# Performance work log

Hardware: AMD Instinct MI355X
Metric: run time of the kernel (lower is better)

Reference implementation:

```python
import jax, jax.numpy as jnp
import numpy as np

IN_FEATURES = 1024
HIDDEN_DIM = 1024
B, S = 4, 4096


def setup_inputs() -> dict:
    key = jax.random.key(0)
    ks = jax.random.split(key, 7)
    lim = 1.0 / np.sqrt(IN_FEATURES)
    x = jax.random.normal(ks[0], (B, S, IN_FEATURES), dtype=jnp.float32)
    Wq = jax.random.uniform(ks[1], (IN_FEATURES, HIDDEN_DIM), jnp.float32, -lim, lim)
    bq = jax.random.uniform(ks[2], (HIDDEN_DIM,), jnp.float32, -lim, lim)
    Wk = jax.random.uniform(ks[3], (IN_FEATURES, HIDDEN_DIM), jnp.float32, -lim, lim)
    bk = jax.random.uniform(ks[4], (HIDDEN_DIM,), jnp.float32, -lim, lim)
    Wv = jax.random.uniform(ks[5], (IN_FEATURES, HIDDEN_DIM), jnp.float32, -lim, lim)
    bv = jax.random.uniform(ks[6], (HIDDEN_DIM,), jnp.float32, -lim, lim)
    return {"x": x, "Wq": Wq, "bq": bq, "Wk": Wk, "bk": bk, "Wv": Wv, "bv": bv}


def reference(x, Wq, bq, Wk, bk, Wv, bv):
    # QKV projections: [B, S, H]
    q = jnp.einsum('bsf,fh->bsh', x, Wq) + bq
    k = jnp.einsum('bsf,fh->bsh', x, Wk) + bk
    v = jnp.einsum('bsf,fh->bsh', x, Wv) + bv
    scale = 1.0 / jnp.sqrt(jnp.asarray(q.shape[-1], dtype=q.dtype))
    scores = jnp.einsum('bqh,bkh->bqk', q, k) * scale  # [B, S, S]
    weights = jax.nn.softmax(scores, axis=-1)
    return jnp.einsum('bqk,bkh->bqh', weights, v)
```

## Files before the change

kernel.cpp:

```cpp
#include <hip/hip_runtime.h>

typedef _Float16 half_t;
typedef _Float16 half4_t __attribute__((ext_vector_type(4)));
typedef _Float16 half8_t __attribute__((ext_vector_type(8)));
typedef float float4_t __attribute__((ext_vector_type(4)));

#define S_LEN 4096
#define NB 4
#define H_DIM 1024

#define MFMA16(a, b, c) __builtin_amdgcn_mfma_f32_16x16x32_f16(a, b, c, 0, 0, 0)

#define BAR_LDS()                                      \
  do {                                                 \
    asm volatile("s_waitcnt lgkmcnt(0)" ::: "memory"); \
    __builtin_amdgcn_s_barrier();                      \
  } while (0)

__global__ __launch_bounds__(256) void wt_prep(
    const float* __restrict__ Wq, const float* __restrict__ Wk,
    const float* __restrict__ Wv, half_t* __restrict__ wth,
    half_t* __restrict__ wtl) {
  const int zi = blockIdx.z;
  const float* W = (zi == 0) ? Wq : (zi == 1) ? Wk : Wv;
  half_t* oh = wth + (size_t)zi * H_DIM * H_DIM;
  half_t* ol = wtl + (size_t)zi * H_DIM * H_DIM;
  const int h0 = blockIdx.x * 32, f0 = blockIdx.y * 32;
  __shared__ float Ws[32][33];
  const int t = threadIdx.x;
  const int c = t & 31, r8 = t >> 5;
#pragma unroll
  for (int rr = 0; rr < 4; rr++)
    Ws[r8 * 4 + rr][c] = W[(size_t)(f0 + r8 * 4 + rr) * H_DIM + h0 + c];
  __syncthreads();
#pragma unroll
  for (int rr = 0; rr < 4; rr++) {
    int h = r8 * 4 + rr;
    float v = Ws[c][h];
    half_t hi = (half_t)v;
    half_t lo = (half_t)(v - (float)hi);
    oh[(size_t)(h0 + h) * H_DIM + f0 + c] = hi;
    ol[(size_t)(h0 + h) * H_DIM + f0 + c] = lo;
  }
}

#define QKV_BK 64

__global__ __launch_bounds__(512, 2) void qkv_mfma(
    const float* __restrict__ x, const half_t* __restrict__ wth,
    const half_t* __restrict__ wtl, const float* __restrict__ bq,
    const float* __restrict__ bk, const float* __restrict__ bv,
    half_t* __restrict__ ws) {
  const int bx = blockIdx.x;
  const int zi = bx >> 2;
  const int m0 = (bx & 3) * 256;
  const int n0 = blockIdx.y * 256;
  const half_t* Ah_g = wth + (size_t)zi * H_DIM * H_DIM;
  const half_t* Al_g = wtl + (size_t)zi * H_DIM * H_DIM;
  const float* bias = (zi == 0) ? bq : (zi == 1) ? bk : bv;
  half_t* out = ws + (size_t)zi * ((size_t)NB * S_LEN * H_DIM);
  const int t = threadIdx.x;
  const int w = t >> 6, lane = t & 63, ln = lane & 15, quad = lane >> 4;

  __shared__ half_t Bs[2][32768];

  float4_t acc[2][16] = {};

  const int ss = t >> 1;
  const int fh = (t & 1) * 32;
  const int snt = ss >> 4, sln = ss & 15;

  const float* xrow = x + (size_t)(n0 + ss) * H_DIM + fh;

  float4 xr[8];
#pragma unroll
  for (int g = 0; g < 4; g++) {
    xr[2 * g] = *(const float4*)(xrow + g * 8);
    xr[2 * g + 1] = *(const float4*)(xrow + g * 8 + 4);
  }
#pragma unroll
  for (int g = 0; g < 4; g++) {
    float vv[8] = {xr[2 * g].x,     xr[2 * g].y,     xr[2 * g].z,
                   xr[2 * g].w,     xr[2 * g + 1].x, xr[2 * g + 1].y,
                   xr[2 * g + 1].z, xr[2 * g + 1].w};
    half8_t hhi, hlo;
#pragma unroll
    for (int j = 0; j < 8; j++) {
      half_t h = (half_t)vv[j];
      hhi[j] = h;
      hlo[j] = (half_t)(vv[j] - (float)h);
    }
    int f = fh + g * 8;
    int k2 = f >> 5, qd = (f >> 3) & 3;
    int base = ((k2 * 16 + snt) * 64 + qd * 16 + sln) * 8;
    *(half8_t*)&Bs[0][base] = hhi;
    *(half8_t*)&Bs[0][16384 + base] = hlo;
  }

  for (int it = 0; it < 16; it++) {
    const int k0 = it * QKV_BK;
    const int cur = it & 1;
    const bool more = (it < 15);

    half8_t ah[2][2], al[2][2];
#pragma unroll
    for (int i = 0; i < 2; i++) {
      const size_t arow =
          (size_t)(m0 + w * 32 + i * 16 + ln) * H_DIM + k0 + quad * 8;
#pragma unroll
      for (int k2 = 0; k2 < 2; k2++) {
        ah[i][k2] = *(const half8_t*)(Ah_g + arow + k2 * 32);
        al[i][k2] = *(const half8_t*)(Al_g + arow + k2 * 32);
      }
    }
    if (more) {
      const float* xp = xrow + (k0 + QKV_BK);
#pragma unroll
      for (int g = 0; g < 4; g++) {
        xr[2 * g] = *(const float4*)(xp + g * 8);
        xr[2 * g + 1] = *(const float4*)(xp + g * 8 + 4);
      }
    }

    BAR_LDS();

#pragma unroll
    for (int k2 = 0; k2 < 2; k2++) {
#pragma unroll
      for (int nt = 0; nt < 16; nt++) {
        int base = ((k2 * 16 + nt) * 64 + lane) * 8;
        half8_t bh = *(const half8_t*)&Bs[cur][base];
        half8_t bl = *(const half8_t*)&Bs[cur][16384 + base];
        acc[0][nt] = MFMA16(ah[0][k2], bh, acc[0][nt]);
        acc[1][nt] = MFMA16(ah[1][k2], bh, acc[1][nt]);
        acc[0][nt] = MFMA16(al[0][k2], bh, acc[0][nt]);
        acc[1][nt] = MFMA16(al[1][k2], bh, acc[1][nt]);
        acc[0][nt] = MFMA16(ah[0][k2], bl, acc[0][nt]);
        acc[1][nt] = MFMA16(ah[1][k2], bl, acc[1][nt]);
      }
    }

    if (more) {
#pragma unroll
      for (int g = 0; g < 4; g++) {
        float vv[8] = {xr[2 * g].x,     xr[2 * g].y,     xr[2 * g].z,
                       xr[2 * g].w,     xr[2 * g + 1].x, xr[2 * g + 1].y,
                       xr[2 * g + 1].z, xr[2 * g + 1].w};
        half8_t hhi, hlo;
#pragma unroll
        for (int j = 0; j < 8; j++) {
          half_t h = (half_t)vv[j];
          hhi[j] = h;
          hlo[j] = (half_t)(vv[j] - (float)h);
        }
        int f = fh + g * 8;
        int k2 = f >> 5, qd = (f >> 3) & 3;
        int base = ((k2 * 16 + snt) * 64 + qd * 16 + sln) * 8;
        *(half8_t*)&Bs[cur ^ 1][base] = hhi;
        *(half8_t*)&Bs[cur ^ 1][16384 + base] = hlo;
      }
    }
  }

  const float oscale = (zi == 0) ? 0.03125f : 1.0f;
  float bb[2][4];
#pragma unroll
  for (int i = 0; i < 2; i++)
#pragma unroll
    for (int r = 0; r < 4; r++)
      bb[i][r] = bias[m0 + w * 32 + i * 16 + quad * 4 + r];

  if (zi < 2) {
#pragma unroll
    for (int i = 0; i < 2; i++)
#pragma unroll
      for (int nt = 0; nt < 16; nt++) {
        half4_t h4;
#pragma unroll
        for (int r = 0; r < 4; r++)
          h4[r] = (half_t)((acc[i][nt][r] + bb[i][r]) * oscale);
        size_t s = n0 + nt * 16 + ln;
        *(half4_t*)&out[s * H_DIM + m0 + w * 32 + i * 16 + quad * 4] = h4;
      }
  } else {
#pragma unroll
    for (int i = 0; i < 2; i++)
#pragma unroll
      for (int nt = 0; nt < 16; nt++) {
        int sf = n0 + nt * 16 + ln;
        int b = sf >> 12, si = sf & 4095;
#pragma unroll
        for (int r = 0; r < 4; r++) {
          int h = m0 + w * 32 + i * 16 + quad * 4 + r;
          out[((size_t)b * H_DIM + h) * S_LEN + si] =
              (half_t)(acc[i][nt][r] + bb[i][r]);
        }
      }
  }
}

#define TQ 64
#define TK 128

__global__ __launch_bounds__(512, 2) void flash_attn(
    const half_t* __restrict__ qw, const half_t* __restrict__ kw,
    const half_t* __restrict__ vt, float* __restrict__ out) {
  const int slot = blockIdx.x & 7;
  const int b = slot >> 1;
  const int qb = ((blockIdx.x >> 3) << 1) | (slot & 1);
  const int q0 = qb * TQ;
  const int t = threadIdx.x;
  const int w = t >> 6;
  const int lane = t & 63;
  const int ln = lane & 15;
  const int quad = lane >> 4;

  __shared__ half_t Qs[65536];
  __shared__ half_t Ps[8192];
  __shared__ float wmax[8][64];
  __shared__ float wl[8][64];

  const half_t* qp = qw + ((size_t)b * S_LEN + q0) * H_DIM;
  const half_t* kbp = kw + (size_t)b * S_LEN * H_DIM;
  const half_t* vbt = vt + (size_t)b * H_DIM * S_LEN;

  const half_t* kr = kbp + (size_t)(w * 16 + ln) * H_DIM + quad * 8;
  half8_t kbuf[6];
#pragma unroll
  for (int d = 0; d < 6; d++) kbuf[d] = *(const half8_t*)(kr + d * 32);

#pragma unroll
  for (int i = 0; i < 16; i++) {
    int flat = t * 8 + i * 4096;
    int r = flat >> 10, c = flat & 1023;
    int rs = r >> 4, lq = r & 15, ks = c >> 5, qd = (c >> 3) & 3;
    *(half8_t*)&Qs[((rs * 32 + ks) * 64 + qd * 16 + lq) * 8] =
        *(const half8_t*)&qp[(size_t)r * H_DIM + c];
  }
  BAR_LDS();

  float m_l = -1e30f;
  float l_l = 0.0f;

  float4_t O[4][8] = {};

  for (int kt = 0; kt < S_LEN; kt += TK) {
    float4_t s[4] = {};
    __builtin_amdgcn_s_setprio(1);
#pragma unroll
    for (int ks = 0; ks < 32; ks++) {
      half8_t a0 = *(const half8_t*)&Qs[(ks * 64 + lane) * 8];
      half8_t a1 = *(const half8_t*)&Qs[16384 + (ks * 64 + lane) * 8];
      half8_t a2 = *(const half8_t*)&Qs[32768 + (ks * 64 + lane) * 8];
      half8_t a3 = *(const half8_t*)&Qs[49152 + (ks * 64 + lane) * 8];
      half8_t kc = kbuf[ks % 6];
      if (ks < 26) kbuf[ks % 6] = *(const half8_t*)(kr + (ks + 6) * 32);
      s[0] = MFMA16(a0, kc, s[0]);
      s[1] = MFMA16(a1, kc, s[1]);
      s[2] = MFMA16(a2, kc, s[2]);
      s[3] = MFMA16(a3, kc, s[3]);
    }
    __builtin_amdgcn_s_setprio(0);

    kr += (size_t)TK * H_DIM;
    if (kt + TK < S_LEN) {
#pragma unroll
      for (int d = 0; d < 6; d++) kbuf[d] = *(const half8_t*)(kr + d * 32);
    }

    const half_t* vbase = vbt + (size_t)(w * 128 + ln) * S_LEN + kt + quad * 8;
    half8_t vr[4];
#pragma unroll
    for (int j = 0; j < 4; j++)
      vr[j] = *(const half8_t*)(vbase + (size_t)j * 16 * S_LEN);

    float rm[4][4];
#pragma unroll
    for (int rs = 0; rs < 4; rs++)
#pragma unroll
      for (int r = 0; r < 4; r++) rm[rs][r] = s[rs][r];
#pragma unroll
    for (int off = 1; off < 16; off <<= 1)
#pragma unroll
      for (int rs = 0; rs < 4; rs++)
#pragma unroll
        for (int r = 0; r < 4; r++)
          rm[rs][r] = fmaxf(rm[rs][r], __shfl_xor(rm[rs][r], off));
    if (ln == 0)
#pragma unroll
      for (int rs = 0; rs < 4; rs++)
#pragma unroll
        for (int r = 0; r < 4; r++)
          wmax[w][rs * 16 + quad * 4 + r] = rm[rs][r];
    BAR_LDS();

    float nm_l = m_l;
#pragma unroll
    for (int w2 = 0; w2 < 8; w2++) nm_l = fmaxf(nm_l, wmax[w2][lane]);
    float aS_l = __expf(m_l - nm_l);
    m_l = nm_l;

    const int pbase = (w >> 1) * 512 + (w & 1) * 256 + (ln >> 3) * 128 +
                      quad * 32 + (ln & 7);
    float pl[4][4];
#pragma unroll
    for (int rs = 0; rs < 4; rs++)
#pragma unroll
      for (int r = 0; r < 4; r++) {
        const int q = rs * 16 + quad * 4 + r;
        float nmq = __shfl(m_l, q);
        float aq = __shfl(aS_l, q);
        float p = __expf(s[rs][r] - nmq);
        pl[rs][r] = p;
        Ps[pbase + rs * 2048 + r * 8] = (half_t)p;
#pragma unroll
        for (int j = 0; j < 8; j++) O[rs][j][r] *= aq;
      }
#pragma unroll
    for (int off = 1; off < 16; off <<= 1)
#pragma unroll
      for (int rs = 0; rs < 4; rs++)
#pragma unroll
        for (int r = 0; r < 4; r++) pl[rs][r] += __shfl_xor(pl[rs][r], off);
    if (ln == 0)
#pragma unroll
      for (int rs = 0; rs < 4; rs++)
#pragma unroll
        for (int r = 0; r < 4; r++)
          wl[w][rs * 16 + quad * 4 + r] = pl[rs][r];
    BAR_LDS();

    float s8_l = 0.f;
#pragma unroll
    for (int w2 = 0; w2 < 8; w2++) s8_l += wl[w2][lane];
    l_l = l_l * aS_l + s8_l;

#pragma unroll
    for (int kc = 0; kc < 4; kc++) {
      half8_t pa[4];
#pragma unroll
      for (int rs = 0; rs < 4; rs++)
        pa[rs] = *(const half8_t*)&Ps[((rs * 4 + kc) * 64 + lane) * 8];
      __builtin_amdgcn_s_setprio(1);
#pragma unroll
      for (int j = 0; j < 8; j++) {
        half8_t vc = vr[j & 3];
        const int jn = j + 4;
        if (jn < 8) {
          vr[j & 3] =
              *(const half8_t*)(vbase + (size_t)jn * 16 * S_LEN + kc * 32);
        } else if (kc < 3) {
          vr[j & 3] = *(const half8_t*)(vbase + (size_t)(jn - 8) * 16 * S_LEN +
                                        (kc + 1) * 32);
        }
#pragma unroll
        for (int rs = 0; rs < 4; rs++)
          O[rs][j] = MFMA16(pa[rs], vc, O[rs][j]);
      }
      __builtin_amdgcn_s_setprio(0);
    }
  }

  float il[4][4];
#pragma unroll
  for (int rs = 0; rs < 4; rs++)
#pragma unroll
    for (int r = 0; r < 4; r++)
      il[rs][r] = 1.0f / __shfl(l_l, rs * 16 + quad * 4 + r);
  float* ob = out + ((size_t)b * S_LEN + q0) * H_DIM + w * 128 + ln;
#pragma unroll
  for (int rs = 0; rs < 4; rs++)
#pragma unroll
    for (int j = 0; j < 8; j++)
#pragma unroll
      for (int r = 0; r < 4; r++)
        ob[(size_t)(rs * 16 + quad * 4 + r) * H_DIM + j * 16] =
            O[rs][j][r] * il[rs][r];
}

extern "C" void kernel_launch(void* const* d_in, const int* in_sizes, int n_in,
                              void* d_out, int out_size, void* d_ws,
                              size_t ws_size, hipStream_t stream) {
  const float* x = (const float*)d_in[0];
  const float* Wq = (const float*)d_in[1];
  const float* bq = (const float*)d_in[2];
  const float* Wk = (const float*)d_in[3];
  const float* bk = (const float*)d_in[4];
  const float* Wv = (const float*)d_in[5];
  const float* bv = (const float*)d_in[6];
  half_t* ws = (half_t*)d_ws;
  float* out = (float*)d_out;

  half_t* wth = (half_t*)d_out;
  half_t* wtl = wth + (size_t)3 * H_DIM * H_DIM;

  wt_prep<<<dim3(32, 32, 3), 256, 0, stream>>>(Wq, Wk, Wv, wth, wtl);

  qkv_mfma<<<dim3(12, 64), 512, 0, stream>>>(x, wth, wtl, bq, bk, bv, ws);

  const half_t* qw = ws;
  const half_t* kw = ws + (size_t)NB * S_LEN * H_DIM;
  const half_t* vt = ws + 2 * (size_t)NB * S_LEN * H_DIM;
  flash_attn<<<dim3((S_LEN / TQ) * NB), 512, 0, stream>>>(qw, kw, vt, out);
}
```

Measured before the change: 957.4 us.

## Stage V-transpose stores through LDS and pace attention blocks with a soft global barrier

The V projection epilogue now writes its tile into shared memory and reads it back so each thread stores 16-byte contiguous runs of the transposed V. The old path wrote scattered 2-byte elements. The attention kernel also adds a loose cross-block pacing point: every 512 keys, thread 0 takes an atomic ticket and spins briefly until its group of 256 blocks catches up. This keeps blocks in step so K/V tiles are shared in L2. It adds a memset, atomic traffic and bounded spin time, and it relies on scratch space inside the output buffer.

Result: slower. 994.6 us (+3.9%).

```diff
diff --git a/kernel.cpp b/kernel.cpp
--- a/kernel.cpp
+++ b/kernel.cpp
@@ -183,19 +183,28 @@
         *(half4_t*)&out[s * H_DIM + m0 + w * 32 + i * 16 + quad * 4] = h4;
       }
   } else {
-#pragma unroll
-    for (int i = 0; i < 2; i++)
-#pragma unroll
-      for (int nt = 0; nt < 16; nt++) {
-        int sf = n0 + nt * 16 + ln;
-        int b = sf >> 12, si = sf & 4095;
-#pragma unroll
-        for (int r = 0; r < 4; r++) {
-          int h = m0 + w * 32 + i * 16 + quad * 4 + r;
-          out[((size_t)b * H_DIM + h) * S_LEN + si] =
+    half_t* BsT = &Bs[0][0];
+    const int bti = n0 >> 12;
+    const int sb = n0 & (S_LEN - 1);
+#pragma unroll
+    for (int i = 0; i < 2; i++) {
+      BAR_LDS();
+#pragma unroll
+      for (int nt = 0; nt < 16; nt++)
+#pragma unroll
+        for (int r = 0; r < 4; r++)
+          BsT[(w * 16 + quad * 4 + r) * 264 + nt * 16 + ln] =
               (half_t)(acc[i][nt][r] + bb[i][r]);
-        }
-      }
+      BAR_LDS();
+#pragma unroll
+      for (int c2 = 0; c2 < 8; c2++) {
+        int idx = c2 * 512 + t;
+        int rl = idx >> 5, ch = idx & 31;
+        half8_t v = *(half8_t*)&BsT[rl * 264 + ch * 8];
+        int h = m0 + (rl >> 4) * 32 + i * 16 + (rl & 15);
+        *(half8_t*)&out[((size_t)bti * H_DIM + h) * S_LEN + sb + ch * 8] = v;
+      }
+    }
   }
 }
 
@@ -204,7 +213,8 @@
 
 __global__ __launch_bounds__(512, 2) void flash_attn(
     const half_t* __restrict__ qw, const half_t* __restrict__ kw,
-    const half_t* __restrict__ vt, float* __restrict__ out) {
+    const half_t* __restrict__ vt, unsigned* __restrict__ pace,
+    float* __restrict__ out) {
   const int slot = blockIdx.x & 7;
   const int b = slot >> 1;
   const int qb = ((blockIdx.x >> 3) << 1) | (slot & 1);
@@ -358,6 +368,18 @@
           O[rs][j] = MFMA16(pa[rs], vc, O[rs][j]);
       }
       __builtin_amdgcn_s_setprio(0);
+    }
+
+    if ((((kt >> 7) & 3) == 3) && (kt + TK < S_LEN)) {
+      if (t == 0) {
+        unsigned ticket = atomicAdd(pace, 1u);
+        unsigned target = ((ticket >> 8) + 1u) << 8;
+        int spin = 0;
+        while (__hip_atomic_load(pace, __ATOMIC_RELAXED,
+                                 __HIP_MEMORY_SCOPE_AGENT) < target &&
+               spin < 300)
+          spin++;
+      }
     }
   }
 
@@ -394,12 +416,17 @@
   half_t* wth = (half_t*)d_out;
   half_t* wtl = wth + (size_t)3 * H_DIM * H_DIM;
 
+  unsigned* pace = (unsigned*)((char*)d_out + (size_t)48 * 1024 * 1024);
+
   wt_prep<<<dim3(32, 32, 3), 256, 0, stream>>>(Wq, Wk, Wv, wth, wtl);
 
   qkv_mfma<<<dim3(12, 64), 512, 0, stream>>>(x, wth, wtl, bq, bk, bv, ws);
+
+  hipMemsetAsync(pace, 0, sizeof(unsigned), stream);
 
   const half_t* qw = ws;
   const half_t* kw = ws + (size_t)NB * S_LEN * H_DIM;
   const half_t* vt = ws + 2 * (size_t)NB * S_LEN * H_DIM;
-  flash_attn<<<dim3((S_LEN / TQ) * NB), 512, 0, stream>>>(qw, kw, vt, out);
+  flash_attn<<<dim3((S_LEN / TQ) * NB), 512, 0, stream>>>(qw, kw, vt, pace,
+                                                          out);
 }
```
